# Performance work log

Hardware: AMD Instinct MI355X
Metric: run time of the kernel (lower is better)

The kernel has to match this reference:

```python
import jax, jax.numpy as jnp
import numpy as np

N_NODES = 50000
N_EDGES = 800000
IN_NODE = 128
IN_EDGE = 64
HEADS = 8
OUT_DIM = 8
HID = HEADS * OUT_DIM


def setup_inputs() -> dict:
    key = jax.random.key(0)
    ks = jax.random.split(key, 12)
    s = 1.0 / np.sqrt(IN_NODE)
    se = 1.0 / np.sqrt(IN_EDGE)
    return {
        "edge_index": jax.random.randint(ks[0], (2, N_EDGES), 0, N_NODES, dtype=jnp.int64),
        "h": jax.random.normal(ks[1], (N_NODES, IN_NODE), dtype=jnp.float32),
        "e": jax.random.normal(ks[2], (N_EDGES, IN_EDGE), dtype=jnp.float32),
        "WQ": jax.random.normal(ks[3], (IN_NODE, HID), dtype=jnp.float32) * s,
        "bQ": jnp.zeros((HID,), dtype=jnp.float32),
        "WK": jax.random.normal(ks[4], (IN_NODE, HID), dtype=jnp.float32) * s,
        "bK": jnp.zeros((HID,), dtype=jnp.float32),
        "WV": jax.random.normal(ks[5], (IN_NODE, HID), dtype=jnp.float32) * s,
        "bV": jnp.zeros((HID,), dtype=jnp.float32),
        "We": jax.random.normal(ks[6], (IN_EDGE, HID), dtype=jnp.float32) * se,
        "be": jnp.zeros((HID,), dtype=jnp.float32),
    }


def reference(edge_index, h, e, WQ, bQ, WK, bK, WV, bV, We, be):
    n = h.shape[0]
    # node projections -> [N, H, D]
    Q = (h @ WQ + bQ).reshape(-1, HEADS, OUT_DIM)
    K = (h @ WK + bK).reshape(-1, HEADS, OUT_DIM)
    V = (h @ WV + bV).reshape(-1, HEADS, OUT_DIM)
    pe = (e @ We + be).reshape(-1, HEADS, OUT_DIM)  # [E, H, D]

    src = edge_index[0]
    dst = edge_index[1]

    # per-edge attention score: K[src] * Q[dst] / sqrt(D) + proj_e
    score = (K[src] * Q[dst]) / np.sqrt(OUT_DIM) + pe  # [E, H, D]
    e_out = score
    a = jnp.exp(jnp.clip(score.sum(-1, keepdims=True), -5.0, 5.0))  # [E, H, 1]

    # scatter-sum of weighted V and scatter-mean of attention weights (by src)
    wV = jax.ops.segment_sum(V[src] * a, src, num_segments=n)       # [N, H, D]
    z_sum = jax.ops.segment_sum(a, src, num_segments=n)             # [N, H, 1]
    cnt = jax.ops.segment_sum(jnp.ones((src.shape[0],), a.dtype), src, num_segments=n)
    z = z_sum / jnp.maximum(cnt, 1.0)[:, None, None]                # scatter-mean

    h_out = wV / (z + 1e-06)
    return (h_out, e_out)
```

## Files before the change

### kernel.cpp

```cpp
#include <hip/hip_runtime.h>
#include <hip/hip_bf16.h>

typedef float        f32x4  __attribute__((ext_vector_type(4)));
typedef short        bf16x8 __attribute__((ext_vector_type(8)));
typedef unsigned int u32x4  __attribute__((ext_vector_type(4)));

#define HEADS 8
#define HID 64
#define IN_NODE 128
#define IN_EDGE 64
#define LDSP 69

static __device__ __forceinline__ short f2bf(float f) {
    unsigned u = __builtin_bit_cast(unsigned, f);
    unsigned r = (u + 0x7FFFu + ((u >> 16) & 1u)) >> 16;
    return (short)r;
}
static __device__ __forceinline__ float bflo(unsigned u) {
    return __builtin_bit_cast(float, u << 16);
}
static __device__ __forceinline__ float bfhi(unsigned u) {
    return __builtin_bit_cast(float, u & 0xFFFF0000u);
}

__global__ __launch_bounds__(256, 4) void qkv_kernel(
    const float* __restrict__ h,
    const float* __restrict__ WQ, const float* __restrict__ bQ,
    const float* __restrict__ WK, const float* __restrict__ bK,
    const float* __restrict__ WV, const float* __restrict__ bV,
    unsigned short* __restrict__ Qb, unsigned short* __restrict__ Kb,
    float* __restrict__ V, int n_nodes)
{
    const int lane = threadIdx.x & 63;
    const int r16  = lane & 15;
    const int g4   = lane >> 4;
    const int wave   = blockIdx.x * (blockDim.x >> 6) + (threadIdx.x >> 6);
    const int nwaves = gridDim.x * (blockDim.x >> 6);
    const int mat  = blockIdx.y;

    const float* __restrict__ W  = (mat == 0) ? WQ : (mat == 1) ? WK : WV;
    const float* __restrict__ bp = (mat == 0) ? bQ : (mat == 1) ? bK : bV;

    bf16x8 bfr[4][4];
#pragma unroll
    for (int ct = 0; ct < 4; ++ct)
#pragma unroll
        for (int kc = 0; kc < 4; ++kc)
#pragma unroll
            for (int j = 0; j < 8; ++j) {
                int k = kc * 32 + g4 * 8 + j;
                bfr[ct][kc][j] = f2bf(W[k * HID + ct * 16 + r16]);
            }
    float bias[4];
#pragma unroll
    for (int ct = 0; ct < 4; ++ct) bias[ct] = bp[ct * 16 + r16];

    const float SC = 0.35355339059327373f;
    const int ntiles = (n_nodes + 15) >> 4;
    for (int tile = wave; tile < ntiles; tile += nwaves) {
        const int row0 = tile * 16;
        int arow = row0 + r16; if (arow > n_nodes - 1) arow = n_nodes - 1;
        const float* ap = h + (size_t)arow * IN_NODE + g4 * 8;

        bf16x8 afr[4];
#pragma unroll
        for (int kc = 0; kc < 4; ++kc) {
            f32x4 p0 = *reinterpret_cast<const f32x4*>(ap + kc * 32);
            f32x4 p1 = *reinterpret_cast<const f32x4*>(ap + kc * 32 + 4);
            afr[kc][0] = f2bf(p0.x); afr[kc][1] = f2bf(p0.y);
            afr[kc][2] = f2bf(p0.z); afr[kc][3] = f2bf(p0.w);
            afr[kc][4] = f2bf(p1.x); afr[kc][5] = f2bf(p1.y);
            afr[kc][6] = f2bf(p1.z); afr[kc][7] = f2bf(p1.w);
        }

        f32x4 acc[4] = {};
#pragma unroll
        for (int ct = 0; ct < 4; ++ct)
#pragma unroll
            for (int kc = 0; kc < 4; ++kc)
                acc[ct] = __builtin_amdgcn_mfma_f32_16x16x32_bf16(
                    afr[kc], bfr[ct][kc], acc[ct], 0, 0, 0);

#pragma unroll
        for (int ct = 0; ct < 4; ++ct)
#pragma unroll
            for (int r = 0; r < 4; ++r) {
                int orow = row0 + g4 * 4 + r;
                if (orow < n_nodes) {
                    float val = acc[ct][r] + bias[ct];
                    size_t idx = (size_t)orow * HID + ct * 16 + r16;
                    if (mat == 0)      Qb[idx] = (unsigned short)f2bf(val);
                    else if (mat == 1) Kb[idx] = (unsigned short)f2bf(val * SC);
                    else               V[idx]  = val;
                }
            }
    }
}

__global__ __launch_bounds__(256, 3) void edge_kernel(
    const int* __restrict__ ei, const float* __restrict__ e,
    const float* __restrict__ We, const float* __restrict__ be,
    const unsigned short* __restrict__ Qb, const unsigned short* __restrict__ Kb,
    float* __restrict__ e_out, float* __restrict__ z_sum,
    float* __restrict__ cnt, int n_edges, int tpw)
{
    const int lane = threadIdx.x & 63;
    const int wid  = threadIdx.x >> 6;
    const int r16  = lane & 15;
    const int g4   = lane >> 4;
    const int el   = lane >> 2;
    const int qg   = lane & 3;

    __shared__ float plds[4][2][16][LDSP];

    const int wave = blockIdx.x * 4 + wid;

    bf16x8 bfr[4][2];
#pragma unroll
    for (int ct = 0; ct < 4; ++ct)
#pragma unroll
        for (int kc = 0; kc < 2; ++kc)
#pragma unroll
            for (int j = 0; j < 8; ++j) {
                int k = kc * 32 + g4 * 8 + j;
                bfr[ct][kc][j] = f2bf(We[k * HID + ct * 16 + r16]);
            }
    float bias[4];
#pragma unroll
    for (int ct = 0; ct < 4; ++ct) bias[ct] = be[ct * 16 + r16];

    const int ntiles = (n_edges + 15) >> 4;
    int t0 = wave * tpw;
    int t1 = t0 + tpw; if (t1 > ntiles) t1 = ntiles;

    for (int t = t0; t < t1; t += 2) {
        f32x4 ev[2][4];
        int srcs[2], dsts[2];
        u32x4 kb[2][2], qb[2][2];
#pragma unroll
        for (int u = 0; u < 2; ++u) {
            int tt = t + u; if (tt > ntiles - 1) tt = ntiles - 1;
            int arow = tt * 16 + r16; if (arow > n_edges - 1) arow = n_edges - 1;
            const float* ap = e + (size_t)arow * IN_EDGE + g4 * 8;
            ev[u][0] = *reinterpret_cast<const f32x4*>(ap);
            ev[u][1] = *reinterpret_cast<const f32x4*>(ap + 4);
            ev[u][2] = *reinterpret_cast<const f32x4*>(ap + 32);
            ev[u][3] = *reinterpret_cast<const f32x4*>(ap + 36);

            int erc = tt * 16 + el; if (erc > n_edges - 1) erc = n_edges - 1;
            srcs[u] = ei[erc];
            dsts[u] = ei[n_edges + erc];
            const unsigned int* kp = reinterpret_cast<const unsigned int*>(Kb)
                                     + (size_t)srcs[u] * 32 + qg * 8;
            const unsigned int* qp = reinterpret_cast<const unsigned int*>(Qb)
                                     + (size_t)dsts[u] * 32 + qg * 8;
            kb[u][0] = *reinterpret_cast<const u32x4*>(kp);
            kb[u][1] = *reinterpret_cast<const u32x4*>(kp + 4);
            qb[u][0] = *reinterpret_cast<const u32x4*>(qp);
            qb[u][1] = *reinterpret_cast<const u32x4*>(qp + 4);
        }

#pragma unroll
        for (int u = 0; u < 2; ++u) {
            bf16x8 afr[2];
            afr[0][0] = f2bf(ev[u][0].x); afr[0][1] = f2bf(ev[u][0].y);
            afr[0][2] = f2bf(ev[u][0].z); afr[0][3] = f2bf(ev[u][0].w);
            afr[0][4] = f2bf(ev[u][1].x); afr[0][5] = f2bf(ev[u][1].y);
            afr[0][6] = f2bf(ev[u][1].z); afr[0][7] = f2bf(ev[u][1].w);
            afr[1][0] = f2bf(ev[u][2].x); afr[1][1] = f2bf(ev[u][2].y);
            afr[1][2] = f2bf(ev[u][2].z); afr[1][3] = f2bf(ev[u][2].w);
            afr[1][4] = f2bf(ev[u][3].x); afr[1][5] = f2bf(ev[u][3].y);
            afr[1][6] = f2bf(ev[u][3].z); afr[1][7] = f2bf(ev[u][3].w);

            f32x4 acc[4] = {};
#pragma unroll
            for (int ct = 0; ct < 4; ++ct) {
                acc[ct] = __builtin_amdgcn_mfma_f32_16x16x32_bf16(afr[0], bfr[ct][0], acc[ct], 0, 0, 0);
                acc[ct] = __builtin_amdgcn_mfma_f32_16x16x32_bf16(afr[1], bfr[ct][1], acc[ct], 0, 0, 0);
            }
#pragma unroll
            for (int ct = 0; ct < 4; ++ct)
#pragma unroll
                for (int r = 0; r < 4; ++r)
                    plds[wid][u][g4 * 4 + r][ct * 16 + r16] = acc[ct][r] + bias[ct];
        }

        asm volatile("s_waitcnt lgkmcnt(0)" ::: "memory");

#pragma unroll
        for (int u = 0; u < 2; ++u) {
            const int tt = t + u;
            const int erow = tt * 16 + el;
            const bool valid = (tt < t1) && (erow < n_edges);

            const float* mrow = &plds[wid][u][el][qg * 16];
            f32x4 p0 = *reinterpret_cast<const f32x4*>(mrow);
            f32x4 p1 = *reinterpret_cast<const f32x4*>(mrow + 4);
            f32x4 p2 = *reinterpret_cast<const f32x4*>(mrow + 8);
            f32x4 p3 = *reinterpret_cast<const f32x4*>(mrow + 12);
            float pe[16];
            pe[0]=p0.x; pe[1]=p0.y; pe[2]=p0.z; pe[3]=p0.w;
            pe[4]=p1.x; pe[5]=p1.y; pe[6]=p1.z; pe[7]=p1.w;
            pe[8]=p2.x; pe[9]=p2.y; pe[10]=p2.z; pe[11]=p2.w;
            pe[12]=p3.x; pe[13]=p3.y; pe[14]=p3.z; pe[15]=p3.w;

            float sc[16];
#pragma unroll
            for (int half = 0; half < 2; ++half)
#pragma unroll
                for (int w = 0; w < 4; ++w) {
                    unsigned ku = kb[u][half][w];
                    unsigned qu = qb[u][half][w];
                    int c = half * 8 + 2 * w;
                    sc[c]     = fmaf(bflo(ku), bflo(qu), pe[c]);
                    sc[c + 1] = fmaf(bfhi(ku), bfhi(qu), pe[c + 1]);
                }

            if (valid) {
                float* op = e_out + (size_t)erow * HID + qg * 16;
                f32x4 s0 = {sc[0], sc[1], sc[2], sc[3]};
                f32x4 s1 = {sc[4], sc[5], sc[6], sc[7]};
                f32x4 s2 = {sc[8], sc[9], sc[10], sc[11]};
                f32x4 s3 = {sc[12], sc[13], sc[14], sc[15]};
                *reinterpret_cast<f32x4*>(op)      = s0;
                *reinterpret_cast<f32x4*>(op + 4)  = s1;
                *reinterpret_cast<f32x4*>(op + 8)  = s2;
                *reinterpret_cast<f32x4*>(op + 12) = s3;
            }

            float hs0 = ((sc[0] + sc[1]) + (sc[2] + sc[3])) + ((sc[4] + sc[5]) + (sc[6] + sc[7]));
            float hs1 = ((sc[8] + sc[9]) + (sc[10] + sc[11])) + ((sc[12] + sc[13]) + (sc[14] + sc[15]));
            float a0 = __expf(fminf(fmaxf(hs0, -5.0f), 5.0f));
            float a1 = __expf(fminf(fmaxf(hs1, -5.0f), 5.0f));
            if (valid) {
                atomicAdd(&z_sum[srcs[u] * HEADS + qg * 2], a0);
                atomicAdd(&z_sum[srcs[u] * HEADS + qg * 2 + 1], a1);
                if (qg == 0) atomicAdd(&cnt[srcs[u]], 1.0f);
            }
        }
    }
}

__global__ __launch_bounds__(256) void finalize_kernel(
    const float* __restrict__ V, const float* __restrict__ z_sum,
    const float* __restrict__ cnt, float* __restrict__ h_out, int total)
{
    int i = blockIdx.x * 256 + threadIdx.x;
    if (i >= total) return;
    int node = i >> 6;
    int head = (i >> 3) & 7;
    float S = z_sum[node * HEADS + head];
    float c = fmaxf(cnt[node], 1.0f);
    h_out[i] = V[i] * S / (S / c + 1e-6f);
}

extern "C" void kernel_launch(void* const* d_in, const int* in_sizes, int n_in,
                              void* d_out, int out_size, void* d_ws, size_t ws_size,
                              hipStream_t stream)
{
    const int*   ei = (const int*)d_in[0];
    const float* h  = (const float*)d_in[1];
    const float* e  = (const float*)d_in[2];
    const float* WQ = (const float*)d_in[3];
    const float* bQ = (const float*)d_in[4];
    const float* WK = (const float*)d_in[5];
    const float* bK = (const float*)d_in[6];
    const float* WV = (const float*)d_in[7];
    const float* bV = (const float*)d_in[8];
    const float* We = (const float*)d_in[9];
    const float* be = (const float*)d_in[10];

    const int n_nodes = in_sizes[1] / IN_NODE;
    const int n_edges = in_sizes[2] / IN_EDGE;

    float* out_h = (float*)d_out;
    float* out_e = out_h + (size_t)n_nodes * HID;

    unsigned short* Qb = (unsigned short*)d_ws;
    unsigned short* Kb = Qb + (size_t)n_nodes * HID;
    float* V     = (float*)(Kb + (size_t)n_nodes * HID);
    float* z_sum = V + (size_t)n_nodes * HID;
    float* cnt   = z_sum + (size_t)n_nodes * HEADS;

    (void)hipMemsetAsync(z_sum, 0, (size_t)n_nodes * (HEADS + 1) * sizeof(float), stream);

    {
        dim3 grid(96, 3);
        qkv_kernel<<<grid, 256, 0, stream>>>(h, WQ, bQ, WK, bK, WV, bV,
                                             Qb, Kb, V, n_nodes);
    }
    {
        const int nblk = 2500;
        const int nwaves = nblk * 4;
        const int ntiles = (n_edges + 15) >> 4;
        const int tpw = (ntiles + nwaves - 1) / nwaves;
        edge_kernel<<<nblk, 256, 0, stream>>>(ei, e, We, be, Qb, Kb,
                                              out_e, z_sum, cnt, n_edges, tpw);
    }
    {
        const int total = n_nodes * HID;
        finalize_kernel<<<(total + 255) / 256, 256, 0, stream>>>(V, z_sum, cnt,
                                                                 out_h, total);
    }
}
```

Baseline: 222.3 us.

## Swap MFMA operands to drop LDS transpose and software-pipeline edge loads

```diff
diff --git a/kernel.cpp b/kernel.cpp
--- a/kernel.cpp
+++ b/kernel.cpp
@@ -3,13 +3,12 @@
 
 typedef float        f32x4  __attribute__((ext_vector_type(4)));
 typedef short        bf16x8 __attribute__((ext_vector_type(8)));
-typedef unsigned int u32x4  __attribute__((ext_vector_type(4)));
+typedef unsigned int u32x2  __attribute__((ext_vector_type(2)));
 
 #define HEADS 8
 #define HID 64
 #define IN_NODE 128
 #define IN_EDGE 64
-#define LDSP 69
 
 static __device__ __forceinline__ short f2bf(float f) {
     unsigned u = __builtin_bit_cast(unsigned, f);
@@ -108,12 +107,12 @@
     const int wid  = threadIdx.x >> 6;
     const int r16  = lane & 15;
     const int g4   = lane >> 4;
-    const int el   = lane >> 2;
-    const int qg   = lane & 3;
-
-    __shared__ float plds[4][2][16][LDSP];
-
-    const int wave = blockIdx.x * 4 + wid;
+
+    const int wave   = blockIdx.x * 4 + wid;
+    const int ntiles = (n_edges + 15) >> 4;
+    int t0 = wave * tpw;
+    int t1 = t0 + tpw; if (t1 > ntiles) t1 = ntiles;
+    if (t0 >= t1) return;
 
     bf16x8 bfr[4][2];
 #pragma unroll
@@ -125,119 +124,118 @@
                 int k = kc * 32 + g4 * 8 + j;
                 bfr[ct][kc][j] = f2bf(We[k * HID + ct * 16 + r16]);
             }
-    float bias[4];
-#pragma unroll
-    for (int ct = 0; ct < 4; ++ct) bias[ct] = be[ct * 16 + r16];
-
-    const int ntiles = (n_edges + 15) >> 4;
-    int t0 = wave * tpw;
-    int t1 = t0 + tpw; if (t1 > ntiles) t1 = ntiles;
-
-    for (int t = t0; t < t1; t += 2) {
-        f32x4 ev[2][4];
-        int srcs[2], dsts[2];
-        u32x4 kb[2][2], qb[2][2];
-#pragma unroll
-        for (int u = 0; u < 2; ++u) {
-            int tt = t + u; if (tt > ntiles - 1) tt = ntiles - 1;
-            int arow = tt * 16 + r16; if (arow > n_edges - 1) arow = n_edges - 1;
+    f32x4 biasf[4];
+#pragma unroll
+    for (int ct = 0; ct < 4; ++ct)
+        biasf[ct] = *reinterpret_cast<const f32x4*>(be + ct * 16 + g4 * 4);
+
+    const unsigned* Kbu = reinterpret_cast<const unsigned*>(Kb);
+    const unsigned* Qbu = reinterpret_cast<const unsigned*>(Qb);
+
+    f32x4 evC[4], evN[4];
+    u32x2 kkC[4], qqC[4], kkN[4], qqN[4];
+    int sC, dC, sN, dN, sN2, dN2;
+
+    {
+        int erc = t0 * 16 + r16; if (erc > n_edges - 1) erc = n_edges - 1;
+        sC = ei[erc]; dC = ei[n_edges + erc];
+        int arow = erc;
+        const float* ap = e + (size_t)arow * IN_EDGE + g4 * 8;
+        evC[0] = __builtin_nontemporal_load(reinterpret_cast<const f32x4*>(ap));
+        evC[1] = __builtin_nontemporal_load(reinterpret_cast<const f32x4*>(ap + 4));
+        evC[2] = __builtin_nontemporal_load(reinterpret_cast<const f32x4*>(ap + 32));
+        evC[3] = __builtin_nontemporal_load(reinterpret_cast<const f32x4*>(ap + 36));
+
+        int tn = (t0 + 1 < t1) ? t0 + 1 : t1 - 1;
+        int ern = tn * 16 + r16; if (ern > n_edges - 1) ern = n_edges - 1;
+        sN = ei[ern]; dN = ei[n_edges + ern];
+
+        const unsigned* kp = Kbu + (size_t)sC * 32 + g4 * 2;
+        const unsigned* qp = Qbu + (size_t)dC * 32 + g4 * 2;
+#pragma unroll
+        for (int ct = 0; ct < 4; ++ct) {
+            kkC[ct] = *reinterpret_cast<const u32x2*>(kp + ct * 8);
+            qqC[ct] = *reinterpret_cast<const u32x2*>(qp + ct * 8);
+        }
+    }
+
+    for (int t = t0; t < t1; ++t) {
+        {
+            int tn2 = (t + 2 < t1) ? t + 2 : t1 - 1;
+            int ern = tn2 * 16 + r16; if (ern > n_edges - 1) ern = n_edges - 1;
+            sN2 = ei[ern]; dN2 = ei[n_edges + ern];
+        }
+        {
+            const unsigned* kp = Kbu + (size_t)sN * 32 + g4 * 2;
+            const unsigned* qp = Qbu + (size_t)dN * 32 + g4 * 2;
+#pragma unroll
+            for (int ct = 0; ct < 4; ++ct) {
+                kkN[ct] = *reinterpret_cast<const u32x2*>(kp + ct * 8);
+                qqN[ct] = *reinterpret_cast<const u32x2*>(qp + ct * 8);
+            }
+        }
+        {
+            int tn = (t + 1 < t1) ? t + 1 : t1 - 1;
+            int arow = tn * 16 + r16; if (arow > n_edges - 1) arow = n_edges - 1;
             const float* ap = e + (size_t)arow * IN_EDGE + g4 * 8;
-            ev[u][0] = *reinterpret_cast<const f32x4*>(ap);
-            ev[u][1] = *reinterpret_cast<const f32x4*>(ap + 4);
-            ev[u][2] = *reinterpret_cast<const f32x4*>(ap + 32);
-            ev[u][3] = *reinterpret_cast<const f32x4*>(ap + 36);
-
-            int erc = tt * 16 + el; if (erc > n_edges - 1) erc = n_edges - 1;
-            srcs[u] = ei[erc];
-            dsts[u] = ei[n_edges + erc];
-            const unsigned int* kp = reinterpret_cast<const unsigned int*>(Kb)
-                                     + (size_t)srcs[u] * 32 + qg * 8;
-            const unsigned int* qp = reinterpret_cast<const unsigned int*>(Qb)
-                                     + (size_t)dsts[u] * 32 + qg * 8;
-            kb[u][0] = *reinterpret_cast<const u32x4*>(kp);
-            kb[u][1] = *reinterpret_cast<const u32x4*>(kp + 4);
-            qb[u][0] = *reinterpret_cast<const u32x4*>(qp);
-            qb[u][1] = *reinterpret_cast<const u32x4*>(qp + 4);
-        }
-
-#pragma unroll
-        for (int u = 0; u < 2; ++u) {
-            bf16x8 afr[2];
-            afr[0][0] = f2bf(ev[u][0].x); afr[0][1] = f2bf(ev[u][0].y);
-            afr[0][2] = f2bf(ev[u][0].z); afr[0][3] = f2bf(ev[u][0].w);
-            afr[0][4] = f2bf(ev[u][1].x); afr[0][5] = f2bf(ev[u][1].y);
-            afr[0][6] = f2bf(ev[u][1].z); afr[0][7] = f2bf(ev[u][1].w);
-            afr[1][0] = f2bf(ev[u][2].x); afr[1][1] = f2bf(ev[u][2].y);
-            afr[1][2] = f2bf(ev[u][2].z); afr[1][3] = f2bf(ev[u][2].w);
-            afr[1][4] = f2bf(ev[u][3].x); afr[1][5] = f2bf(ev[u][3].y);
-            afr[1][6] = f2bf(ev[u][3].z); afr[1][7] = f2bf(ev[u][3].w);
-
-            f32x4 acc[4] = {};
+            evN[0] = __builtin_nontemporal_load(reinterpret_cast<const f32x4*>(ap));
+            evN[1] = __builtin_nontemporal_load(reinterpret_cast<const f32x4*>(ap + 4));
+            evN[2] = __builtin_nontemporal_load(reinterpret_cast<const f32x4*>(ap + 32));
+            evN[3] = __builtin_nontemporal_load(reinterpret_cast<const f32x4*>(ap + 36));
+        }
+
+        bf16x8 afr[2];
+        afr[0][0] = f2bf(evC[0].x); afr[0][1] = f2bf(evC[0].y);
+        afr[0][2] = f2bf(evC[0].z); afr[0][3] = f2bf(evC[0].w);
+        afr[0][4] = f2bf(evC[1].x); afr[0][5] = f2bf(evC[1].y);
+        afr[0][6] = f2bf(evC[1].z); afr[0][7] = f2bf(evC[1].w);
+        afr[1][0] = f2bf(evC[2].x); afr[1][1] = f2bf(evC[2].y);
+        afr[1][2] = f2bf(evC[2].z); afr[1][3] = f2bf(evC[2].w);
+        afr[1][4] = f2bf(evC[3].x); afr[1][5] = f2bf(evC[3].y);
+        afr[1][6] = f2bf(evC[3].z); afr[1][7] = f2bf(evC[3].w);
+
+        f32x4 acc[4];
+#pragma unroll
+        for (int ct = 0; ct < 4; ++ct) {
+            acc[ct] = biasf[ct];
+            acc[ct] = __builtin_amdgcn_mfma_f32_16x16x32_bf16(bfr[ct][0], afr[0], acc[ct], 0, 0, 0);
+            acc[ct] = __builtin_amdgcn_mfma_f32_16x16x32_bf16(bfr[ct][1], afr[1], acc[ct], 0, 0, 0);
+        }
+
+        const int erow = t * 16 + r16;
+        const bool valid = erow < n_edges;
+        float hsum[4];
+#pragma unroll
+        for (int ct = 0; ct < 4; ++ct) {
+            float s0 = fmaf(bflo(kkC[ct].x), bflo(qqC[ct].x), acc[ct][0]);
+            float s1 = fmaf(bfhi(kkC[ct].x), bfhi(qqC[ct].x), acc[ct][1]);
+            float s2 = fmaf(bflo(kkC[ct].y), bflo(qqC[ct].y), acc[ct][2]);
+            float s3 = fmaf(bfhi(kkC[ct].y), bfhi(qqC[ct].y), acc[ct][3]);
+            if (valid) {
+                f32x4 sv = {s0, s1, s2, s3};
+                *reinterpret_cast<f32x4*>(e_out + (size_t)erow * HID + ct * 16 + g4 * 4) = sv;
+            }
+            hsum[ct] = (s0 + s1) + (s2 + s3);
+        }
+#pragma unroll
+        for (int ct = 0; ct < 4; ++ct)
+            hsum[ct] += __shfl_xor(hsum[ct], 16);
+        if (valid && (lane & 16) == 0) {
+            const int hb = g4 >> 1;
 #pragma unroll
             for (int ct = 0; ct < 4; ++ct) {
-                acc[ct] = __builtin_amdgcn_mfma_f32_16x16x32_bf16(afr[0], bfr[ct][0], acc[ct], 0, 0, 0);
-                acc[ct] = __builtin_amdgcn_mfma_f32_16x16x32_bf16(afr[1], bfr[ct][1], acc[ct], 0, 0, 0);
-            }
-#pragma unroll
-            for (int ct = 0; ct < 4; ++ct)
-#pragma unroll
-                for (int r = 0; r < 4; ++r)
-                    plds[wid][u][g4 * 4 + r][ct * 16 + r16] = acc[ct][r] + bias[ct];
-        }
-
-        asm volatile("s_waitcnt lgkmcnt(0)" ::: "memory");
-
-#pragma unroll
-        for (int u = 0; u < 2; ++u) {
-            const int tt = t + u;
-            const int erow = tt * 16 + el;
-            const bool valid = (tt < t1) && (erow < n_edges);
-
-            const float* mrow = &plds[wid][u][el][qg * 16];
-            f32x4 p0 = *reinterpret_cast<const f32x4*>(mrow);
-            f32x4 p1 = *reinterpret_cast<const f32x4*>(mrow + 4);
-            f32x4 p2 = *reinterpret_cast<const f32x4*>(mrow + 8);
-            f32x4 p3 = *reinterpret_cast<const f32x4*>(mrow + 12);
-            float pe[16];
-            pe[0]=p0.x; pe[1]=p0.y; pe[2]=p0.z; pe[3]=p0.w;
-            pe[4]=p1.x; pe[5]=p1.y; pe[6]=p1.z; pe[7]=p1.w;
-            pe[8]=p2.x; pe[9]=p2.y; pe[10]=p2.z; pe[11]=p2.w;
-            pe[12]=p3.x; pe[13]=p3.y; pe[14]=p3.z; pe[15]=p3.w;
-
-            float sc[16];
-#pragma unroll
-            for (int half = 0; half < 2; ++half)
-#pragma unroll
-                for (int w = 0; w < 4; ++w) {
-                    unsigned ku = kb[u][half][w];
-                    unsigned qu = qb[u][half][w];
-                    int c = half * 8 + 2 * w;
-                    sc[c]     = fmaf(bflo(ku), bflo(qu), pe[c]);
-                    sc[c + 1] = fmaf(bfhi(ku), bfhi(qu), pe[c + 1]);
-                }
-
-            if (valid) {
-                float* op = e_out + (size_t)erow * HID + qg * 16;
-                f32x4 s0 = {sc[0], sc[1], sc[2], sc[3]};
-                f32x4 s1 = {sc[4], sc[5], sc[6], sc[7]};
-                f32x4 s2 = {sc[8], sc[9], sc[10], sc[11]};
-                f32x4 s3 = {sc[12], sc[13], sc[14], sc[15]};
-                *reinterpret_cast<f32x4*>(op)      = s0;
-                *reinterpret_cast<f32x4*>(op + 4)  = s1;
-                *reinterpret_cast<f32x4*>(op + 8)  = s2;
-                *reinterpret_cast<f32x4*>(op + 12) = s3;
-            }
-
-            float hs0 = ((sc[0] + sc[1]) + (sc[2] + sc[3])) + ((sc[4] + sc[5]) + (sc[6] + sc[7]));
-            float hs1 = ((sc[8] + sc[9]) + (sc[10] + sc[11])) + ((sc[12] + sc[13]) + (sc[14] + sc[15]));
-            float a0 = __expf(fminf(fmaxf(hs0, -5.0f), 5.0f));
-            float a1 = __expf(fminf(fmaxf(hs1, -5.0f), 5.0f));
-            if (valid) {
-                atomicAdd(&z_sum[srcs[u] * HEADS + qg * 2], a0);
-                atomicAdd(&z_sum[srcs[u] * HEADS + qg * 2 + 1], a1);
-                if (qg == 0) atomicAdd(&cnt[srcs[u]], 1.0f);
-            }
-        }
+                float a = __expf(fminf(fmaxf(hsum[ct], -5.0f), 5.0f));
+                atomicAdd(&z_sum[sC * HEADS + 2 * ct + hb], a);
+            }
+        }
+        if (valid && g4 == 0) atomicAdd(&cnt[sC], 1.0f);
+
+#pragma unroll
+        for (int i = 0; i < 4; ++i) {
+            evC[i] = evN[i];
+            kkC[i] = kkN[i]; qqC[i] = qqN[i];
+        }
+        sC = sN; dC = dN; sN = sN2; dN = dN2;
     }
 }
 
@@ -290,7 +288,7 @@
                                              Qb, Kb, V, n_nodes);
     }
     {
-        const int nblk = 2500;
+        const int nblk = 768;
         const int nwaves = nblk * 4;
         const int ntiles = (n_edges + 15) >> 4;
         const int tpw = (ntiles + nwaves - 1) / nwaves;
```

After: 273.2 us. +22.9%, slower.

## Software-pipeline edge feature and index loads, use nontemporal loads, retune grids

Applied to the files above, without the earlier changes.

```diff
diff --git a/kernel.cpp b/kernel.cpp
--- a/kernel.cpp
+++ b/kernel.cpp
@@ -114,6 +114,10 @@
     __shared__ float plds[4][2][16][LDSP];
 
     const int wave = blockIdx.x * 4 + wid;
+    const int ntiles = (n_edges + 15) >> 4;
+    int t0 = wave * tpw;
+    int t1 = t0 + tpw; if (t1 > ntiles) t1 = ntiles;
+    if (t0 >= t1) return;
 
     bf16x8 bfr[4][2];
 #pragma unroll
@@ -129,48 +133,66 @@
 #pragma unroll
     for (int ct = 0; ct < 4; ++ct) bias[ct] = be[ct * 16 + r16];
 
-    const int ntiles = (n_edges + 15) >> 4;
-    int t0 = wave * tpw;
-    int t1 = t0 + tpw; if (t1 > ntiles) t1 = ntiles;
+    const unsigned* Kbu = reinterpret_cast<const unsigned*>(Kb);
+    const unsigned* Qbu = reinterpret_cast<const unsigned*>(Qb);
+
+    f32x4 evC[2][4], evN[2][4];
+    int srcC[2], dstC[2], srcN[2], dstN[2];
+
+#pragma unroll
+    for (int u = 0; u < 2; ++u) {
+        int tt = t0 + u; if (tt > ntiles - 1) tt = ntiles - 1;
+        int arow = tt * 16 + r16; if (arow > n_edges - 1) arow = n_edges - 1;
+        const float* ap = e + (size_t)arow * IN_EDGE + g4 * 8;
+        evC[u][0] = __builtin_nontemporal_load(reinterpret_cast<const f32x4*>(ap));
+        evC[u][1] = __builtin_nontemporal_load(reinterpret_cast<const f32x4*>(ap + 4));
+        evC[u][2] = __builtin_nontemporal_load(reinterpret_cast<const f32x4*>(ap + 32));
+        evC[u][3] = __builtin_nontemporal_load(reinterpret_cast<const f32x4*>(ap + 36));
+        int erc = tt * 16 + el; if (erc > n_edges - 1) erc = n_edges - 1;
+        srcC[u] = ei[erc];
+        dstC[u] = ei[n_edges + erc];
+    }
 
     for (int t = t0; t < t1; t += 2) {
-        f32x4 ev[2][4];
-        int srcs[2], dsts[2];
         u32x4 kb[2][2], qb[2][2];
 #pragma unroll
         for (int u = 0; u < 2; ++u) {
-            int tt = t + u; if (tt > ntiles - 1) tt = ntiles - 1;
-            int arow = tt * 16 + r16; if (arow > n_edges - 1) arow = n_edges - 1;
-            const float* ap = e + (size_t)arow * IN_EDGE + g4 * 8;
-            ev[u][0] = *reinterpret_cast<const f32x4*>(ap);
-            ev[u][1] = *reinterpret_cast<const f32x4*>(ap + 4);
-            ev[u][2] = *reinterpret_cast<const f32x4*>(ap + 32);
-            ev[u][3] = *reinterpret_cast<const f32x4*>(ap + 36);
-
-            int erc = tt * 16 + el; if (erc > n_edges - 1) erc = n_edges - 1;
-            srcs[u] = ei[erc];
-            dsts[u] = ei[n_edges + erc];
-            const unsigned int* kp = reinterpret_cast<const unsigned int*>(Kb)
-                                     + (size_t)srcs[u] * 32 + qg * 8;
-            const unsigned int* qp = reinterpret_cast<const unsigned int*>(Qb)
-                                     + (size_t)dsts[u] * 32 + qg * 8;
+            const unsigned* kp = Kbu + (size_t)srcC[u] * 32 + qg * 8;
+            const unsigned* qp = Qbu + (size_t)dstC[u] * 32 + qg * 8;
             kb[u][0] = *reinterpret_cast<const u32x4*>(kp);
             kb[u][1] = *reinterpret_cast<const u32x4*>(kp + 4);
             qb[u][0] = *reinterpret_cast<const u32x4*>(qp);
             qb[u][1] = *reinterpret_cast<const u32x4*>(qp + 4);
         }
 
+        {
+            int tn = t + 2; if (tn > t1 - 1) tn = t1 - 1;
+#pragma unroll
+            for (int u = 0; u < 2; ++u) {
+                int tt = tn + u; if (tt > ntiles - 1) tt = ntiles - 1;
+                int arow = tt * 16 + r16; if (arow > n_edges - 1) arow = n_edges - 1;
+                const float* ap = e + (size_t)arow * IN_EDGE + g4 * 8;
+                evN[u][0] = __builtin_nontemporal_load(reinterpret_cast<const f32x4*>(ap));
+                evN[u][1] = __builtin_nontemporal_load(reinterpret_cast<const f32x4*>(ap + 4));
+                evN[u][2] = __builtin_nontemporal_load(reinterpret_cast<const f32x4*>(ap + 32));
+                evN[u][3] = __builtin_nontemporal_load(reinterpret_cast<const f32x4*>(ap + 36));
+                int erc = tt * 16 + el; if (erc > n_edges - 1) erc = n_edges - 1;
+                srcN[u] = ei[erc];
+                dstN[u] = ei[n_edges + erc];
+            }
+        }
+
 #pragma unroll
         for (int u = 0; u < 2; ++u) {
             bf16x8 afr[2];
-            afr[0][0] = f2bf(ev[u][0].x); afr[0][1] = f2bf(ev[u][0].y);
-            afr[0][2] = f2bf(ev[u][0].z); afr[0][3] = f2bf(ev[u][0].w);
-            afr[0][4] = f2bf(ev[u][1].x); afr[0][5] = f2bf(ev[u][1].y);
-            afr[0][6] = f2bf(ev[u][1].z); afr[0][7] = f2bf(ev[u][1].w);
-            afr[1][0] = f2bf(ev[u][2].x); afr[1][1] = f2bf(ev[u][2].y);
-            afr[1][2] = f2bf(ev[u][2].z); afr[1][3] = f2bf(ev[u][2].w);
-            afr[1][4] = f2bf(ev[u][3].x); afr[1][5] = f2bf(ev[u][3].y);
-            afr[1][6] = f2bf(ev[u][3].z); afr[1][7] = f2bf(ev[u][3].w);
+            afr[0][0] = f2bf(evC[u][0].x); afr[0][1] = f2bf(evC[u][0].y);
+            afr[0][2] = f2bf(evC[u][0].z); afr[0][3] = f2bf(evC[u][0].w);
+            afr[0][4] = f2bf(evC[u][1].x); afr[0][5] = f2bf(evC[u][1].y);
+            afr[0][6] = f2bf(evC[u][1].z); afr[0][7] = f2bf(evC[u][1].w);
+            afr[1][0] = f2bf(evC[u][2].x); afr[1][1] = f2bf(evC[u][2].y);
+            afr[1][2] = f2bf(evC[u][2].z); afr[1][3] = f2bf(evC[u][2].w);
+            afr[1][4] = f2bf(evC[u][3].x); afr[1][5] = f2bf(evC[u][3].y);
+            afr[1][6] = f2bf(evC[u][3].z); afr[1][7] = f2bf(evC[u][3].w);
 
             f32x4 acc[4] = {};
 #pragma unroll
@@ -233,10 +255,17 @@
             float a0 = __expf(fminf(fmaxf(hs0, -5.0f), 5.0f));
             float a1 = __expf(fminf(fmaxf(hs1, -5.0f), 5.0f));
             if (valid) {
-                atomicAdd(&z_sum[srcs[u] * HEADS + qg * 2], a0);
-                atomicAdd(&z_sum[srcs[u] * HEADS + qg * 2 + 1], a1);
-                if (qg == 0) atomicAdd(&cnt[srcs[u]], 1.0f);
-            }
+                atomicAdd(&z_sum[srcC[u] * HEADS + qg * 2], a0);
+                atomicAdd(&z_sum[srcC[u] * HEADS + qg * 2 + 1], a1);
+                if (qg == 0) atomicAdd(&cnt[srcC[u]], 1.0f);
+            }
+        }
+
+#pragma unroll
+        for (int u = 0; u < 2; ++u) {
+#pragma unroll
+            for (int i = 0; i < 4; ++i) evC[u][i] = evN[u][i];
+            srcC[u] = srcN[u]; dstC[u] = dstN[u];
         }
     }
 }
@@ -285,12 +314,12 @@
     (void)hipMemsetAsync(z_sum, 0, (size_t)n_nodes * (HEADS + 1) * sizeof(float), stream);
 
     {
-        dim3 grid(96, 3);
+        dim3 grid(256, 3);
         qkv_kernel<<<grid, 256, 0, stream>>>(h, WQ, bQ, WK, bK, WV, bV,
                                              Qb, Kb, V, n_nodes);
     }
     {
-        const int nblk = 2500;
+        const int nblk = 2048;
         const int nwaves = nblk * 4;
         const int ntiles = (n_edges + 15) >> 4;
         const int tpw = (ntiles + nwaves - 1) / nwaves;
```

Measured after the change: 219.4 us (median of 2 runs). Within noise of the previous version (-1.3%).
